# Optimization experiments

Hardware: AMD Instinct MI355X
Metric: run time of the kernel (lower is better)

Reference implementation:

```python
import jax, jax.numpy as jnp
import numpy as np

H, W, S, C = 1080, 1920, 2000, 8


def setup_inputs() -> dict:
    key = jax.random.key(0)
    k1, k2, k3, k4 = jax.random.split(key, 4)
    # superpixel label map, labels in 1..S (original code uses 1-based labels)
    spx = jax.random.randint(k1, (1, 1, H, W), 1, S + 1, dtype=jnp.int32)
    # per-superpixel KNN class prediction, labels in 1..C
    knn_pred = jax.random.randint(k2, (S,), 1, C + 1, dtype=jnp.int32)
    # per-superpixel per-class KNN distance / kmeans-centroid distance
    knn_dist = jax.random.uniform(k3, (S, C), dtype=jnp.float32)
    cent_dist = jax.random.uniform(k4, (S, C), dtype=jnp.float32)
    return {"spx": spx, "knn_pred": knn_pred, "knn_dist": knn_dist, "cent_dist": cent_dist}


def reference(spx, knn_pred, knn_dist, cent_dist):
    # The original does, for each superpixel i, a boolean-mask scatter:
    #   s = (spx[0,0] == i+1); preseg[s] = knn_pred[i]; knn_att[s] = knn_dist[i]; ...
    # which is equivalent to a single O(H*W) gather indexed by the label map.
    idx = spx[0, 0] - 1                      # [H, W], 0-based superpixel index
    preseg = knn_pred[idx]                   # [H, W]
    knn_att = knn_dist[idx]                  # [H, W, C]
    cent_att = cent_dist[idx]                # [H, W, C]

    num_cls = knn_dist.shape[1]
    neg_inf = jnp.float32(-jnp.inf)
    ams = []
    # contrast maps: for class c (labels 2..num_cls), max over all OTHER class channels
    for c in range(2, num_cls + 1):
        j = c - 1
        keep = jnp.arange(num_cls) != j      # [C]
        knn_contrast = jnp.max(jnp.where(keep, knn_att, neg_inf), axis=2)   # [H, W]
        cent_contrast = jnp.max(jnp.where(keep, cent_att, neg_inf), axis=2)  # [H, W]
        ams.append(jnp.stack([knn_att[..., j], knn_contrast,
                              cent_att[..., j], cent_contrast]))            # [4, H, W]
    attmaps = jnp.stack(ams)                 # [num_cls-1, 4, H, W]
    return preseg[None, None], attmaps
```

## Files before the change

kernel.cpp:

```cpp
#include <hip/hip_runtime.h>

#define H_ 1080
#define W_ 1920
#define S_ 2000
#define C_ 8
#define HW_ (H_*W_)
#define NQ  (HW_/4)
#define ROWF 32

__global__ void build_table_k(const int* __restrict__ knn_pred,
                              const float* __restrict__ knn_dist,
                              const float* __restrict__ cent_dist,
                              float* __restrict__ tab){
  int s = blockIdx.x * blockDim.x + threadIdx.x;
  if (s >= S_) return;
  float kd[C_], cd[C_];
  const float4* kr = reinterpret_cast<const float4*>(knn_dist  + s * C_);
  const float4* cr = reinterpret_cast<const float4*>(cent_dist + s * C_);
  float4 a = kr[0], b = kr[1], c = cr[0], d = cr[1];
  kd[0]=a.x; kd[1]=a.y; kd[2]=a.z; kd[3]=a.w; kd[4]=b.x; kd[5]=b.y; kd[6]=b.z; kd[7]=b.w;
  cd[0]=c.x; cd[1]=c.y; cd[2]=c.z; cd[3]=c.w; cd[4]=d.x; cd[5]=d.y; cd[6]=d.z; cd[7]=d.w;

  float row[ROWF];
  #pragma unroll
  for (int i = 0; i < ROWF; ++i) row[i] = 0.0f;
  row[0] = (float)knn_pred[s];
  #pragma unroll
  for (int j = 1; j < C_; ++j){
    float km = -3.0e38f, cm = -3.0e38f;
    #pragma unroll
    for (int k = 0; k < C_; ++k){
      if (k == j) continue;
      km = fmaxf(km, kd[k]);
      cm = fmaxf(cm, cd[k]);
    }
    int bix = 1 + (j - 1) * 4;
    row[bix + 0] = kd[j];
    row[bix + 1] = km;
    row[bix + 2] = cd[j];
    row[bix + 3] = cm;
  }
  float* g = tab + s * ROWF;
  #pragma unroll
  for (int i = 0; i < ROWF; i += 4)
    *reinterpret_cast<float4*>(g + i) = make_float4(row[i], row[i+1], row[i+2], row[i+3]);
}

__global__ __launch_bounds__(256) void scatter_k(const int* __restrict__ spx,
                                                 const float* __restrict__ tab,
                                                 float* __restrict__ out){
  int t = blockIdx.x * blockDim.x + threadIdx.x;
  int p = t * 4;
  if (p >= HW_) return;
  int4 s4 = *reinterpret_cast<const int4*>(spx + p);
  const float4* r0 = reinterpret_cast<const float4*>(tab + (s4.x - 1) * ROWF);
  const float4* r1 = reinterpret_cast<const float4*>(tab + (s4.y - 1) * ROWF);
  const float4* r2 = reinterpret_cast<const float4*>(tab + (s4.z - 1) * ROWF);
  const float4* r3 = reinterpret_cast<const float4*>(tab + (s4.w - 1) * ROWF);

  float4 a0[8], a1[8], a2[8], a3[8];
  #pragma unroll
  for (int i = 0; i < 8; ++i){ a0[i] = r0[i]; a1[i] = r1[i]; a2[i] = r2[i]; a3[i] = r3[i]; }
  const float* f0 = reinterpret_cast<const float*>(a0);
  const float* f1 = reinterpret_cast<const float*>(a1);
  const float* f2 = reinterpret_cast<const float*>(a2);
  const float* f3 = reinterpret_cast<const float*>(a3);

  #pragma unroll
  for (int m = 0; m < 29; ++m){
    float4 w;
    w.x = f0[m]; w.y = f1[m]; w.z = f2[m]; w.w = f3[m];
    *reinterpret_cast<float4*>(out + (size_t)m * HW_ + p) = w;
  }
}

extern "C" void kernel_launch(void* const* d_in, const int* in_sizes, int n_in,
                              void* d_out, int out_size, void* d_ws, size_t ws_size,
                              hipStream_t stream)
{
  const int*   spx       = (const int*)  d_in[0];
  const int*   knn_pred  = (const int*)  d_in[1];
  const float* knn_dist  = (const float*)d_in[2];
  const float* cent_dist = (const float*)d_in[3];
  float* out = (float*)d_out;
  float* tab = (float*)d_ws;

  build_table_k<<<(S_ + 255) / 256, 256, 0, stream>>>(knn_pred, knn_dist, cent_dist, tab);
  scatter_k<<<NQ / 256, 256, 0, stream>>>(spx, tab, out);
}
```

Baseline: 254.5 us.

## Transpose table per output plane, stage in LDS, compress labels to u16

The lookup table is stored plane-major so each output plane's 2000 values fit in shared memory. A new kernel first compresses the int32 label map to 16-bit indices. The scatter then runs one block per (plane, chunk), loading that plane's table into LDS and gathering from LDS. This replaces the scattered global-memory row gathers. The cost is an extra kernel launch, the label map being re-read once per plane (29 times, though at half size), and LDS bank conflicts on random lookups.

```diff
diff --git a/kernel.cpp b/kernel.cpp
--- a/kernel.cpp
+++ b/kernel.cpp
@@ -6,12 +6,19 @@
 #define C_ 8
 #define HW_ (H_*W_)
 #define NQ  (HW_/4)
-#define ROWF 32
+#define NP  29
+#define TP  2048
+#define BPP 405
+#define QPB 1280
 
-__global__ void build_table_k(const int* __restrict__ knn_pred,
-                              const float* __restrict__ knn_dist,
-                              const float* __restrict__ cent_dist,
-                              float* __restrict__ tab){
+typedef unsigned short u16;
+
+#define IDX_OFF (256*1024)
+
+__global__ void build_tabT_k(const int* __restrict__ knn_pred,
+                             const float* __restrict__ knn_dist,
+                             const float* __restrict__ cent_dist,
+                             float* __restrict__ tabT){
   int s = blockIdx.x * blockDim.x + threadIdx.x;
   if (s >= S_) return;
   float kd[C_], cd[C_];
@@ -21,10 +28,7 @@
   kd[0]=a.x; kd[1]=a.y; kd[2]=a.z; kd[3]=a.w; kd[4]=b.x; kd[5]=b.y; kd[6]=b.z; kd[7]=b.w;
   cd[0]=c.x; cd[1]=c.y; cd[2]=c.z; cd[3]=c.w; cd[4]=d.x; cd[5]=d.y; cd[6]=d.z; cd[7]=d.w;
 
-  float row[ROWF];
-  #pragma unroll
-  for (int i = 0; i < ROWF; ++i) row[i] = 0.0f;
-  row[0] = (float)knn_pred[s];
+  tabT[0 * TP + s] = (float)knn_pred[s];
   #pragma unroll
   for (int j = 1; j < C_; ++j){
     float km = -3.0e38f, cm = -3.0e38f;
@@ -34,43 +38,52 @@
       km = fmaxf(km, kd[k]);
       cm = fmaxf(cm, cd[k]);
     }
-    int bix = 1 + (j - 1) * 4;
-    row[bix + 0] = kd[j];
-    row[bix + 1] = km;
-    row[bix + 2] = cd[j];
-    row[bix + 3] = cm;
+    int m = 1 + (j - 1) * 4;
+    tabT[(m + 0) * TP + s] = kd[j];
+    tabT[(m + 1) * TP + s] = km;
+    tabT[(m + 2) * TP + s] = cd[j];
+    tabT[(m + 3) * TP + s] = cm;
   }
-  float* g = tab + s * ROWF;
-  #pragma unroll
-  for (int i = 0; i < ROWF; i += 4)
-    *reinterpret_cast<float4*>(g + i) = make_float4(row[i], row[i+1], row[i+2], row[i+3]);
 }
 
-__global__ __launch_bounds__(256) void scatter_k(const int* __restrict__ spx,
-                                                 const float* __restrict__ tab,
-                                                 float* __restrict__ out){
+__global__ __launch_bounds__(256) void compress_idx_k(const int* __restrict__ spx,
+                                                      u16* __restrict__ idx16){
   int t = blockIdx.x * blockDim.x + threadIdx.x;
   int p = t * 4;
   if (p >= HW_) return;
   int4 s4 = *reinterpret_cast<const int4*>(spx + p);
-  const float4* r0 = reinterpret_cast<const float4*>(tab + (s4.x - 1) * ROWF);
-  const float4* r1 = reinterpret_cast<const float4*>(tab + (s4.y - 1) * ROWF);
-  const float4* r2 = reinterpret_cast<const float4*>(tab + (s4.z - 1) * ROWF);
-  const float4* r3 = reinterpret_cast<const float4*>(tab + (s4.w - 1) * ROWF);
+  ushort4 v;
+  v.x = (u16)(s4.x - 1); v.y = (u16)(s4.y - 1);
+  v.z = (u16)(s4.z - 1); v.w = (u16)(s4.w - 1);
+  *reinterpret_cast<ushort4*>(idx16 + p) = v;
+}
 
-  float4 a0[8], a1[8], a2[8], a3[8];
+__global__ __launch_bounds__(256) void scatter_k(const u16* __restrict__ idx16,
+                                                 const float* __restrict__ tabT,
+                                                 float* __restrict__ out){
+  __shared__ float lds[TP];
+  const unsigned bid = blockIdx.x;
+  const unsigned m   = bid / BPP;
+  const unsigned cx  = bid % BPP;
+  const unsigned tid = threadIdx.x;
+
+  {
+    const float4* g = reinterpret_cast<const float4*>(tabT + m * TP) + tid * 2;
+    float4 v0 = g[0], v1 = g[1];
+    float4* l = reinterpret_cast<float4*>(lds) + tid * 2;
+    l[0] = v0; l[1] = v1;
+  }
+  __syncthreads();
+
+  const unsigned qbase = cx * QPB;
+  float* op = out + (size_t)m * HW_;
   #pragma unroll
-  for (int i = 0; i < 8; ++i){ a0[i] = r0[i]; a1[i] = r1[i]; a2[i] = r2[i]; a3[i] = r3[i]; }
-  const float* f0 = reinterpret_cast<const float*>(a0);
-  const float* f1 = reinterpret_cast<const float*>(a1);
-  const float* f2 = reinterpret_cast<const float*>(a2);
-  const float* f3 = reinterpret_cast<const float*>(a3);
-
-  #pragma unroll
-  for (int m = 0; m < 29; ++m){
+  for (int it = 0; it < 5; ++it){
+    unsigned q = qbase + it * 256 + tid;
+    ushort4 iv = *reinterpret_cast<const ushort4*>(idx16 + (size_t)q * 4);
     float4 w;
-    w.x = f0[m]; w.y = f1[m]; w.z = f2[m]; w.w = f3[m];
-    *reinterpret_cast<float4*>(out + (size_t)m * HW_ + p) = w;
+    w.x = lds[iv.x]; w.y = lds[iv.y]; w.z = lds[iv.z]; w.w = lds[iv.w];
+    *reinterpret_cast<float4*>(op + (size_t)q * 4) = w;
   }
 }
 
@@ -82,9 +95,11 @@
   const int*   knn_pred  = (const int*)  d_in[1];
   const float* knn_dist  = (const float*)d_in[2];
   const float* cent_dist = (const float*)d_in[3];
-  float* out = (float*)d_out;
-  float* tab = (float*)d_ws;
+  float* out   = (float*)d_out;
+  float* tabT  = (float*)d_ws;
+  u16*   idx16 = (u16*)((char*)d_ws + IDX_OFF);
 
-  build_table_k<<<(S_ + 255) / 256, 256, 0, stream>>>(knn_pred, knn_dist, cent_dist, tab);
-  scatter_k<<<NQ / 256, 256, 0, stream>>>(spx, tab, out);
+  build_tabT_k<<<(S_ + 255) / 256, 256, 0, stream>>>(knn_pred, knn_dist, cent_dist, tabT);
+  compress_idx_k<<<NQ / 256, 256, 0, stream>>>(spx, idx16);
+  scatter_k<<<NP * BPP, 256, 0, stream>>>(idx16, tabT, out);
 }
```

Result: no change. 253.9 us (-0.2%).
